# Performance work log

Hardware: AMD Instinct MI355X
Metric: run time of the kernel (lower is better)

The kernel has to match this reference:

```python
import jax, jax.numpy as jnp
import numpy as np

N = 200000   # nodes
E = 400000   # edges
G = 4096     # graphs in batch
F_IN = 77    # atom feature dim
D = 128      # dim_drug
L = 3        # layer_drug
BN_EPS = 1e-5


def setup_inputs() -> dict:
    key = jax.random.key(0)
    ks = jax.random.split(key, 16)
    inp = {}
    inp["x"] = jax.random.normal(ks[0], (N, F_IN), jnp.float32)
    inp["edge_index"] = jax.random.randint(ks[1], (2, E), 0, N, dtype=jnp.int64)
    inp["batch"] = jnp.sort(jax.random.randint(ks[2], (N,), 0, G, dtype=jnp.int64))
    dims = [F_IN, D, D]
    i = 3
    for l in range(L):
        din = dims[l]
        inp[f"w1_{l}"] = jax.random.normal(ks[i], (din, D), jnp.float32) / np.sqrt(din); i += 1
        inp[f"b1_{l}"] = jnp.zeros((D,), jnp.float32)
        inp[f"w2_{l}"] = jax.random.normal(ks[i], (D, D), jnp.float32) / np.sqrt(D); i += 1
        inp[f"b2_{l}"] = jnp.zeros((D,), jnp.float32)
        inp[f"gamma_{l}"] = jnp.ones((D,), jnp.float32)
        inp[f"beta_{l}"] = jnp.zeros((D,), jnp.float32)
    inp["w_emb"] = jax.random.normal(ks[i], (L * D, 256), jnp.float32) / np.sqrt(L * D)
    inp["b_emb"] = jnp.zeros((256,), jnp.float32)
    return inp


def _gin_bn_layer(h, src, dst, w1, b1, w2, b2, gamma, beta):
    # GINConv (eps=0): out_i = MLP(x_i + sum_{j->i} x_j)
    agg = jax.ops.segment_sum(h[src], dst, num_segments=N)  # scatter-add aggregation
    h = h + agg
    h = jax.nn.relu(h @ w1 + b1) @ w2 + b2                  # GIN MLP
    h = jax.nn.relu(h)                                       # outer F.relu
    mu = jnp.mean(h, axis=0)
    var = jnp.var(h, axis=0)                                  # biased var (training-mode BN)
    return (h - mu) * jax.lax.rsqrt(var + BN_EPS) * gamma + beta


def reference(x, edge_index, batch,
              w1_0, b1_0, w2_0, b2_0, gamma_0, beta_0,
              w1_1, b1_1, w2_1, b2_1, gamma_1, beta_1,
              w1_2, b1_2, w2_2, b2_2, gamma_2, beta_2,
              w_emb, b_emb):
    src, dst = edge_index[0], edge_index[1]
    layers = [(w1_0, b1_0, w2_0, b2_0, gamma_0, beta_0),
              (w1_1, b1_1, w2_1, b2_1, gamma_1, beta_1),
              (w1_2, b1_2, w2_2, b2_2, gamma_2, beta_2)]
    h = x
    outs = []
    for (w1, b1, w2, b2, g, b) in layers:
        h = _gin_bn_layer(h, src, dst, w1, b1, w2, b2, g, b)
        outs.append(h)
    node_rep = jnp.concatenate(outs, axis=1)                  # JK 'cat' -> [N, L*D]
    pooled = jax.ops.segment_max(node_rep, batch, num_segments=G)  # global_max_pool -> [G, L*D]
    # drug_emb: Linear -> ReLU -> Dropout (identity in eval)
    return jax.nn.relu(pooled @ w_emb + b_emb)
```

## Files before the change

### kernel.cpp

```cpp
#include <hip/hip_runtime.h>
#include <hip/hip_bf16.h>
#include <float.h>

#define NN 200000
#define NE 400000
#define NG 4096
#define FIN 77
#define DD 128
#define BN_EPS 1e-5f
#define NB_SCAN ((NN + 255) / 256)
#define NBLK (NN / 64)

typedef float f32x4 __attribute__((ext_vector_type(4)));
typedef short s16x8 __attribute__((ext_vector_type(8)));

__device__ __forceinline__ unsigned short f2bf(float x) {
    unsigned b = __float_as_uint(x);
    unsigned r = (b + 0x7FFFu + ((b >> 16) & 1u)) >> 16;
    return (unsigned short)r;
}
__device__ __forceinline__ float bf2f(unsigned short u) {
    return __uint_as_float(((unsigned)u) << 16);
}

__global__ void detect_kernel(const unsigned* eidx, const unsigned* batch, int* flags) {
    if (threadIdx.x == 0 && blockIdx.x == 0) {
        int e64 = 1, b64 = 1;
        for (int i = 0; i < 16; i++) {
            if (eidx[2 * NE - 1 - 2 * i] != 0u) e64 = 0;
            if (batch[NN - 1 - 2 * i] != 0u) b64 = 0;
        }
        flags[0] = e64;
        flags[1] = b64;
    }
}

__device__ __forceinline__ int load_idx(const void* p, int is64, long long i) {
    return is64 ? (int)((const long long*)p)[i] : ((const int*)p)[i];
}

__global__ void graph_starts_kernel(const void* batch, const int* flags, int* start) {
    int g = blockIdx.x * blockDim.x + threadIdx.x;
    if (g > NG) return;
    int is64 = flags[1];
    int lo = 0, hi = NN;
    while (lo < hi) {
        int mid = (lo + hi) >> 1;
        int v = load_idx(batch, is64, mid);
        if (v < g) lo = mid + 1; else hi = mid;
    }
    start[g] = lo;
}

__global__ void count_kernel(const void* __restrict__ eidx, const int* __restrict__ flags,
                             int* __restrict__ deg) {
    int e = blockIdx.x * 256 + threadIdx.x;
    if (e >= NE) return;
    int dst = load_idx(eidx, flags[0], (long long)NE + e);
    atomicAdd(&deg[dst], 1);
}

__global__ void scan1_kernel(const int* __restrict__ deg, int* __restrict__ incl,
                             int* __restrict__ bsum) {
    __shared__ int sh[256];
    int i = blockIdx.x * 256 + threadIdx.x;
    int v = (i < NN) ? deg[i] : 0;
    sh[threadIdx.x] = v;
    __syncthreads();
    for (int off = 1; off < 256; off <<= 1) {
        int t = (threadIdx.x >= off) ? sh[threadIdx.x - off] : 0;
        __syncthreads();
        sh[threadIdx.x] += t;
        __syncthreads();
    }
    if (i < NN) incl[i] = sh[threadIdx.x];
    if (threadIdx.x == 255) bsum[blockIdx.x] = sh[255];
}

__global__ void scan2_kernel(int* __restrict__ bsum) {
    __shared__ int sh[NB_SCAN];
    for (int i = threadIdx.x; i < NB_SCAN; i += blockDim.x) sh[i] = bsum[i];
    __syncthreads();
    if (threadIdx.x == 0) {
        int acc = 0;
        for (int i = 0; i < NB_SCAN; i++) { int t = sh[i]; sh[i] = acc; acc += t; }
    }
    __syncthreads();
    for (int i = threadIdx.x; i < NB_SCAN; i += blockDim.x) bsum[i] = sh[i];
}

__global__ void scan3_kernel(const int* __restrict__ incl, const int* __restrict__ deg,
                             const int* __restrict__ bsum, int* __restrict__ rowptr,
                             int* __restrict__ cursor) {
    int i = blockIdx.x * 256 + threadIdx.x;
    if (i < NN) {
        int ex = bsum[blockIdx.x] + incl[i] - deg[i];
        rowptr[i] = ex;
        cursor[i] = ex;
    }
    if (i == 0) rowptr[NN] = NE;
}

__global__ void fill_kernel(const void* __restrict__ eidx, const int* __restrict__ flags,
                            int* __restrict__ cursor, int* __restrict__ slots) {
    int e = blockIdx.x * 256 + threadIdx.x;
    if (e >= NE) return;
    int is64 = flags[0];
    int src = load_idx(eidx, is64, e);
    int dst = load_idx(eidx, is64, (long long)NE + e);
    int pos = atomicAdd(&cursor[dst], 1);
    slots[pos] = src;
}

__global__ void xconv_kernel(const float* __restrict__ x, unsigned short* __restrict__ xb) {
    int idx = blockIdx.x * 256 + threadIdx.x;
    int row = idx / 12, c8 = (idx % 12) * 8;
    union { s16x8 v; unsigned short u[8]; } pk;
#pragma unroll
    for (int j = 0; j < 8; j++) {
        int c = c8 + j;
        pk.u[j] = (c < FIN) ? f2bf(x[(long long)row * FIN + c]) : (unsigned short)0;
    }
    *(s16x8*)&xb[(long long)row * 96 + c8] = pk.v;
}

__global__ void wconv_kernel(const float* __restrict__ w1, const float* __restrict__ w2,
                             unsigned short* __restrict__ wt1, unsigned short* __restrict__ wt2,
                             int K1) {
    int idx = blockIdx.x * 256 + threadIdx.x;
    int c = idx >> 7, k = idx & 127;
    wt1[idx] = f2bf(k < K1 ? w1[k * DD + c] : 0.f);
    wt2[idx] = f2bf(w2[k * DD + c]);
}

template <int L0>
__global__ __launch_bounds__(256) void fused_layer(
    const unsigned short* __restrict__ src, const float* __restrict__ ss,
    const int* __restrict__ rowptr, const int* __restrict__ slots,
    const unsigned short* __restrict__ wt1, const unsigned short* __restrict__ wt2,
    const float* __restrict__ b1, const float* __restrict__ b2,
    unsigned short* __restrict__ out, float* __restrict__ partials)
{
    __shared__ unsigned short Xs[64 * 128];
    constexpr int SK = L0 ? 96 : 128;
    constexpr int KS1 = L0 ? 3 : 4;
    int tid = threadIdx.x;
    int lane = tid & 63;
    int w = tid >> 6;
    long long rowBase = (long long)blockIdx.x * 64;

    {
        int rp = tid >> 4;
        int ci = tid & 15;
        int c8 = ci * 8;
        float sc[8], sh[8];
        if (!L0) {
#pragma unroll
            for (int j = 0; j < 8; j++) { sc[j] = ss[c8 + j]; sh[j] = ss[DD + c8 + j]; }
        }
#pragma unroll
        for (int p = 0; p < 4; p++) {
            int r = p * 16 + rp;
            long long gr = rowBase + r;
            float a[8];
            if (L0 && c8 >= 96) {
#pragma unroll
                for (int j = 0; j < 8; j++) a[j] = 0.f;
            } else {
                int lo = rowptr[gr], hi = rowptr[gr + 1];
                s16x8 v = *(const s16x8*)&src[gr * SK + c8];
                if (L0) {
#pragma unroll
                    for (int j = 0; j < 8; j++) a[j] = bf2f((unsigned short)v[j]);
                } else {
#pragma unroll
                    for (int j = 0; j < 8; j++) a[j] = bf2f((unsigned short)v[j]) * sc[j] + sh[j];
                }
                int k = lo;
                for (; k + 1 < hi; k += 2) {
                    long long s0 = slots[k], s1 = slots[k + 1];
                    s16x8 v0 = *(const s16x8*)&src[s0 * SK + c8];
                    s16x8 v1 = *(const s16x8*)&src[s1 * SK + c8];
                    if (L0) {
#pragma unroll
                        for (int j = 0; j < 8; j++)
                            a[j] += bf2f((unsigned short)v0[j]) + bf2f((unsigned short)v1[j]);
                    } else {
#pragma unroll
                        for (int j = 0; j < 8; j++)
                            a[j] += (bf2f((unsigned short)v0[j]) * sc[j] + sh[j]) +
                                    (bf2f((unsigned short)v1[j]) * sc[j] + sh[j]);
                    }
                }
                if (k < hi) {
                    long long s0 = slots[k];
                    s16x8 v0 = *(const s16x8*)&src[s0 * SK + c8];
#pragma unroll
                    for (int j = 0; j < 8; j++) {
                        float f = bf2f((unsigned short)v0[j]);
                        a[j] += L0 ? f : (f * sc[j] + sh[j]);
                    }
                }
            }
            union { s16x8 v; unsigned short u[8]; } pk;
#pragma unroll
            for (int j = 0; j < 8; j++) pk.u[j] = f2bf(a[j]);
            *(s16x8*)&Xs[r * 128 + (c8 ^ ((r & 7) << 3))] = pk.v;
        }
    }

    int colbase = w * 32 + (lane & 15);
    s16x8 w1f[2][4], w2f[2][4];
#pragma unroll
    for (int cb = 0; cb < 2; cb++) {
        int col = colbase + cb * 16;
#pragma unroll
        for (int ks = 0; ks < KS1; ks++)
            w1f[cb][ks] = *(const s16x8*)&wt1[col * 128 + ks * 32 + (lane >> 4) * 8];
#pragma unroll
        for (int ks = 0; ks < 4; ks++)
            w2f[cb][ks] = *(const s16x8*)&wt2[col * 128 + ks * 32 + (lane >> 4) * 8];
    }
    float bs1[2], bs2[2];
#pragma unroll
    for (int cb = 0; cb < 2; cb++) {
        bs1[cb] = b1[colbase + cb * 16];
        bs2[cb] = b2[colbase + cb * 16];
    }

    __syncthreads();

    f32x4 acc[4][2];
#pragma unroll
    for (int rb = 0; rb < 4; rb++)
#pragma unroll
        for (int cb = 0; cb < 2; cb++) acc[rb][cb] = 0;
#pragma unroll
    for (int ks = 0; ks < KS1; ks++) {
        int lk = ks * 32 + (lane >> 4) * 8;
        s16x8 af[4];
#pragma unroll
        for (int rb = 0; rb < 4; rb++) {
            int r = rb * 16 + (lane & 15);
            af[rb] = *(const s16x8*)&Xs[r * 128 + (lk ^ ((r & 7) << 3))];
        }
#pragma unroll
        for (int rb = 0; rb < 4; rb++)
#pragma unroll
            for (int cb = 0; cb < 2; cb++)
                acc[rb][cb] = __builtin_amdgcn_mfma_f32_16x16x32_bf16(af[rb], w1f[cb][ks], acc[rb][cb], 0, 0, 0);
    }

    __syncthreads();

#pragma unroll
    for (int rb = 0; rb < 4; rb++)
#pragma unroll
        for (int cb = 0; cb < 2; cb++) {
            int col = colbase + cb * 16;
#pragma unroll
            for (int reg = 0; reg < 4; reg++) {
                int row = rb * 16 + (lane >> 4) * 4 + reg;
                float v = fmaxf(acc[rb][cb][reg] + bs1[cb], 0.f);
                Xs[row * 128 + (col ^ ((row & 7) << 3))] = f2bf(v);
            }
        }

    __syncthreads();

#pragma unroll
    for (int rb = 0; rb < 4; rb++)
#pragma unroll
        for (int cb = 0; cb < 2; cb++) acc[rb][cb] = 0;
#pragma unroll
    for (int ks = 0; ks < 4; ks++) {
        int lk = ks * 32 + (lane >> 4) * 8;
        s16x8 af[4];
#pragma unroll
        for (int rb = 0; rb < 4; rb++) {
            int r = rb * 16 + (lane & 15);
            af[rb] = *(const s16x8*)&Xs[r * 128 + (lk ^ ((r & 7) << 3))];
        }
#pragma unroll
        for (int rb = 0; rb < 4; rb++)
#pragma unroll
            for (int cb = 0; cb < 2; cb++)
                acc[rb][cb] = __builtin_amdgcn_mfma_f32_16x16x32_bf16(af[rb], w2f[cb][ks], acc[rb][cb], 0, 0, 0);
    }

    float ps[2] = {0.f, 0.f}, pq[2] = {0.f, 0.f};
#pragma unroll
    for (int rb = 0; rb < 4; rb++)
#pragma unroll
        for (int cb = 0; cb < 2; cb++) {
            int col = colbase + cb * 16;
#pragma unroll
            for (int reg = 0; reg < 4; reg++) {
                long long row = rowBase + rb * 16 + (lane >> 4) * 4 + reg;
                float v = fmaxf(acc[rb][cb][reg] + bs2[cb], 0.f);
                unsigned short ub = f2bf(v);
                out[row * DD + col] = ub;
                float vb = bf2f(ub);
                ps[cb] += vb;
                pq[cb] += vb * vb;
            }
        }
#pragma unroll
    for (int cb = 0; cb < 2; cb++) {
        ps[cb] += __shfl_xor(ps[cb], 16); ps[cb] += __shfl_xor(ps[cb], 32);
        pq[cb] += __shfl_xor(pq[cb], 16); pq[cb] += __shfl_xor(pq[cb], 32);
        if (lane < 16) {
            int col = colbase + cb * 16;
            partials[(long long)blockIdx.x * 256 + col] = ps[cb];
            partials[(long long)blockIdx.x * 256 + 128 + col] = pq[cb];
        }
    }
}

__global__ void bn_red2_kernel(const float* __restrict__ partials, float* __restrict__ sums) {
    float s = 0.f;
    for (int b = blockIdx.x; b < NBLK; b += gridDim.x)
        s += partials[(long long)b * 256 + threadIdx.x];
    atomicAdd(&sums[threadIdx.x], s);
}

__global__ void bn_finalize_kernel(const float* __restrict__ sums,
                                   const float* __restrict__ gamma,
                                   const float* __restrict__ beta,
                                   float* __restrict__ ss) {
    int c = threadIdx.x;
    float mu = sums[c] / (float)NN;
    float var = sums[DD + c] / (float)NN - mu * mu;
    float sc = gamma[c] * rsqrtf(var + BN_EPS);
    ss[c] = sc;
    ss[DD + c] = beta[c] - mu * sc;
}

__global__ void pool_kernel(const unsigned short* __restrict__ hm, const float* __restrict__ ss,
                            const int* __restrict__ start, float* __restrict__ pooled, int l) {
    int g = blockIdx.x;
    int c = threadIdx.x;
    int lo = start[g], hi = start[g + 1];
    float sc = ss[c], sh = ss[DD + c];
    float m = -FLT_MAX;
    for (int n = lo; n < hi; n++)
        m = fmaxf(m, bf2f(hm[(long long)n * DD + c]) * sc + sh);
    pooled[(long long)g * (3 * DD) + l * DD + c] = m;
}

__global__ __launch_bounds__(256) void emb_kernel(const float* __restrict__ pooled,
                                                  const float* __restrict__ w,
                                                  const float* __restrict__ b,
                                                  float* __restrict__ out) {
    __shared__ float pl[8][384];
    int tid = threadIdx.x;
    int g0 = blockIdx.x * 8;
#pragma unroll
    for (int i = 0; i < 12; i++) {
        int idx = tid + i * 256;
        int gg = idx / 384, c = idx % 384;
        pl[gg][c] = pooled[(long long)(g0 + gg) * 384 + c];
    }
    __syncthreads();
    float acc[8];
#pragma unroll
    for (int gg = 0; gg < 8; gg++) acc[gg] = 0.f;
    for (int k = 0; k < 384; k++) {
        float wv = w[k * 256 + tid];
#pragma unroll
        for (int gg = 0; gg < 8; gg++) acc[gg] += pl[gg][k] * wv;
    }
    float bb = b[tid];
#pragma unroll
    for (int gg = 0; gg < 8; gg++)
        out[(long long)(g0 + gg) * 256 + tid] = fmaxf(acc[gg] + bb, 0.f);
}

extern "C" void kernel_launch(void* const* d_in, const int* in_sizes, int n_in,
                              void* d_out, int out_size, void* d_ws, size_t ws_size,
                              hipStream_t stream) {
    const float* x = (const float*)d_in[0];
    const void* eidx = d_in[1];
    const void* batch = d_in[2];
    const float* w1[3] = { (const float*)d_in[3],  (const float*)d_in[9],  (const float*)d_in[15] };
    const float* b1[3] = { (const float*)d_in[4],  (const float*)d_in[10], (const float*)d_in[16] };
    const float* w2[3] = { (const float*)d_in[5],  (const float*)d_in[11], (const float*)d_in[17] };
    const float* b2[3] = { (const float*)d_in[6],  (const float*)d_in[12], (const float*)d_in[18] };
    const float* gm[3] = { (const float*)d_in[7],  (const float*)d_in[13], (const float*)d_in[19] };
    const float* bt[3] = { (const float*)d_in[8],  (const float*)d_in[14], (const float*)d_in[20] };
    const float* w_emb = (const float*)d_in[21];
    const float* b_emb = (const float*)d_in[22];
    float* out = (float*)d_out;

    unsigned short* R1 = (unsigned short*)d_ws;
    unsigned short* R2 = R1 + (size_t)NN * DD;
    float* pooled = (float*)(R2 + (size_t)NN * DD);
    float* partials = pooled + (size_t)NG * 384;
    unsigned short* wtb = (unsigned short*)(partials + (size_t)NBLK * 256);
    float* sums = (float*)(wtb + 6 * 16384);
    float* ss = sums + 256;
    int* start = (int*)(ss + 256);
    int* flags = start + NG + 1;
    int* deg = flags + 2;
    int* incl = deg + NN;
    int* bsum = incl + NN;
    int* rowptr = bsum + NB_SCAN;
    int* cursor = rowptr + NN + 1;
    int* slots = cursor + NN;

    detect_kernel<<<1, 64, 0, stream>>>((const unsigned*)eidx, (const unsigned*)batch, flags);
    graph_starts_kernel<<<(NG + 1 + 255) / 256, 256, 0, stream>>>(batch, flags, start);

    hipMemsetAsync(deg, 0, (size_t)NN * sizeof(int), stream);
    count_kernel<<<(NE + 255) / 256, 256, 0, stream>>>(eidx, flags, deg);
    scan1_kernel<<<NB_SCAN, 256, 0, stream>>>(deg, incl, bsum);
    scan2_kernel<<<1, 1024, 0, stream>>>(bsum);
    scan3_kernel<<<NB_SCAN, 256, 0, stream>>>(incl, deg, bsum, rowptr, cursor);
    fill_kernel<<<(NE + 255) / 256, 256, 0, stream>>>(eidx, flags, cursor, slots);

    xconv_kernel<<<(NN * 12) / 256, 256, 0, stream>>>(x, R1);
    for (int l = 0; l < 3; l++)
        wconv_kernel<<<64, 256, 0, stream>>>(w1[l], w2[l], wtb + l * 2 * 16384,
                                             wtb + l * 2 * 16384 + 16384, (l == 0) ? FIN : DD);

    unsigned short* hin[3] = { R1, R2, R1 };
    unsigned short* hout[3] = { R2, R1, R2 };
    for (int l = 0; l < 3; l++) {
        const unsigned short* wt1 = wtb + l * 2 * 16384;
        const unsigned short* wt2 = wt1 + 16384;
        if (l == 0)
            fused_layer<1><<<NBLK, 256, 0, stream>>>(hin[l], ss, rowptr, slots, wt1, wt2,
                                                     b1[l], b2[l], hout[l], partials);
        else
            fused_layer<0><<<NBLK, 256, 0, stream>>>(hin[l], ss, rowptr, slots, wt1, wt2,
                                                     b1[l], b2[l], hout[l], partials);
        hipMemsetAsync(sums, 0, 256 * sizeof(float), stream);
        bn_red2_kernel<<<64, 256, 0, stream>>>(partials, sums);
        bn_finalize_kernel<<<1, 128, 0, stream>>>(sums, gm[l], bt[l], ss);
        pool_kernel<<<NG, 128, 0, stream>>>(hout[l], ss, start, pooled, l);
    }
    emb_kernel<<<NG / 8, 256, 0, stream>>>(pooled, w_emb, b_emb, out);
}
```

Baseline: 438.3 us.

## Fuse global max pooling into layer epilogue via atomic per-graph max/min

Removes the separate pool kernel and graph-start binary search. Each fused layer now tracks per-graph running max, plus min when any gamma is negative, of the post-ReLU bf16 values and merges them with integer atomics. A small finalize kernel then applies the BN affine, picking max or min by the sign of the scale. The last layer skips writing its hidden output since only the pooled values are needed. Aggregation is also changed to sum raw bf16 neighbours and apply the BN affine once, scaled by the neighbour count, and bn_red2 gets more blocks. The cost is extra memsets and atomic traffic per layer.

```diff
diff --git a/kernel.cpp b/kernel.cpp
--- a/kernel.cpp
+++ b/kernel.cpp
@@ -39,17 +39,11 @@
     return is64 ? (int)((const long long*)p)[i] : ((const int*)p)[i];
 }
 
-__global__ void graph_starts_kernel(const void* batch, const int* flags, int* start) {
-    int g = blockIdx.x * blockDim.x + threadIdx.x;
-    if (g > NG) return;
-    int is64 = flags[1];
-    int lo = 0, hi = NN;
-    while (lo < hi) {
-        int mid = (lo + hi) >> 1;
-        int v = load_idx(batch, is64, mid);
-        if (v < g) lo = mid + 1; else hi = mid;
-    }
-    start[g] = lo;
+__global__ void gsign_kernel(const float* ga, const float* gb, const float* gc, int* gneg) {
+    int c = threadIdx.x;
+    if (ga[c] < 0.f) atomicOr(&gneg[0], 1);
+    if (gb[c] < 0.f) atomicOr(&gneg[1], 1);
+    if (gc[c] < 0.f) atomicOr(&gneg[2], 1);
 }
 
 __global__ void count_kernel(const void* __restrict__ eidx, const int* __restrict__ flags,
@@ -133,15 +127,18 @@
     wt2[idx] = f2bf(w2[k * DD + c]);
 }
 
-template <int L0>
+template <int L0, int STOREH>
 __global__ __launch_bounds__(256) void fused_layer(
     const unsigned short* __restrict__ src, const float* __restrict__ ss,
     const int* __restrict__ rowptr, const int* __restrict__ slots,
     const unsigned short* __restrict__ wt1, const unsigned short* __restrict__ wt2,
     const float* __restrict__ b1, const float* __restrict__ b2,
-    unsigned short* __restrict__ out, float* __restrict__ partials)
+    unsigned short* __restrict__ out, float* __restrict__ partials,
+    const int* __restrict__ flags, const void* __restrict__ batch,
+    const int* __restrict__ gneg_l, float* __restrict__ pmax, float* __restrict__ pmin)
 {
     __shared__ unsigned short Xs[64 * 128];
+    __shared__ int gidL[64];
     constexpr int SK = L0 ? 96 : 128;
     constexpr int KS1 = L0 ? 3 : 4;
     int tid = threadIdx.x;
@@ -149,10 +146,11 @@
     int w = tid >> 6;
     long long rowBase = (long long)blockIdx.x * 64;
 
+    if (tid < 64) gidL[tid] = load_idx(batch, flags[1], rowBase + tid);
+
     {
         int rp = tid >> 4;
-        int ci = tid & 15;
-        int c8 = ci * 8;
+        int c8 = (tid & 15) * 8;
         float sc[8], sh[8];
         if (!L0) {
 #pragma unroll
@@ -168,38 +166,27 @@
                 for (int j = 0; j < 8; j++) a[j] = 0.f;
             } else {
                 int lo = rowptr[gr], hi = rowptr[gr + 1];
-                s16x8 v = *(const s16x8*)&src[gr * SK + c8];
-                if (L0) {
-#pragma unroll
-                    for (int j = 0; j < 8; j++) a[j] = bf2f((unsigned short)v[j]);
-                } else {
-#pragma unroll
-                    for (int j = 0; j < 8; j++) a[j] = bf2f((unsigned short)v[j]) * sc[j] + sh[j];
+                int d = hi - lo;
+                long long s0 = (d > 0) ? (long long)slots[lo] : gr;
+                long long s1 = (d > 1) ? (long long)slots[lo + 1] : gr;
+                s16x8 vo = *(const s16x8*)&src[gr * SK + c8];
+                s16x8 v0 = *(const s16x8*)&src[s0 * SK + c8];
+                s16x8 v1 = *(const s16x8*)&src[s1 * SK + c8];
+                float m0 = (d > 0) ? 1.f : 0.f, m1 = (d > 1) ? 1.f : 0.f;
+#pragma unroll
+                for (int j = 0; j < 8; j++)
+                    a[j] = bf2f((unsigned short)vo[j]) + m0 * bf2f((unsigned short)v0[j])
+                                                      + m1 * bf2f((unsigned short)v1[j]);
+                for (int k = lo + 2; k < hi; k++) {
+                    long long sk = slots[k];
+                    s16x8 vk = *(const s16x8*)&src[sk * SK + c8];
+#pragma unroll
+                    for (int j = 0; j < 8; j++) a[j] += bf2f((unsigned short)vk[j]);
                 }
-                int k = lo;
-                for (; k + 1 < hi; k += 2) {
-                    long long s0 = slots[k], s1 = slots[k + 1];
-                    s16x8 v0 = *(const s16x8*)&src[s0 * SK + c8];
-                    s16x8 v1 = *(const s16x8*)&src[s1 * SK + c8];
-                    if (L0) {
-#pragma unroll
-                        for (int j = 0; j < 8; j++)
-                            a[j] += bf2f((unsigned short)v0[j]) + bf2f((unsigned short)v1[j]);
-                    } else {
-#pragma unroll
-                        for (int j = 0; j < 8; j++)
-                            a[j] += (bf2f((unsigned short)v0[j]) * sc[j] + sh[j]) +
-                                    (bf2f((unsigned short)v1[j]) * sc[j] + sh[j]);
-                    }
-                }
-                if (k < hi) {
-                    long long s0 = slots[k];
-                    s16x8 v0 = *(const s16x8*)&src[s0 * SK + c8];
-#pragma unroll
-                    for (int j = 0; j < 8; j++) {
-                        float f = bf2f((unsigned short)v0[j]);
-                        a[j] += L0 ? f : (f * sc[j] + sh[j]);
-                    }
+                if (!L0) {
+                    float cnt = (float)(d + 1);
+#pragma unroll
+                    for (int j = 0; j < 8; j++) a[j] = a[j] * sc[j] + cnt * sh[j];
                 }
             }
             union { s16x8 v; unsigned short u[8]; } pk;
@@ -288,23 +275,39 @@
                 acc[rb][cb] = __builtin_amdgcn_mfma_f32_16x16x32_bf16(af[rb], w2f[cb][ks], acc[rb][cb], 0, 0, 0);
     }
 
+    int gn = gneg_l[0];
     float ps[2] = {0.f, 0.f}, pq[2] = {0.f, 0.f};
 #pragma unroll
-    for (int rb = 0; rb < 4; rb++)
-#pragma unroll
-        for (int cb = 0; cb < 2; cb++) {
-            int col = colbase + cb * 16;
+    for (int cb = 0; cb < 2; cb++) {
+        int col = colbase + cb * 16;
+        int curg = -1;
+        float cmx = 0.f, cmn = 0.f;
+#pragma unroll
+        for (int rb = 0; rb < 4; rb++) {
 #pragma unroll
             for (int reg = 0; reg < 4; reg++) {
-                long long row = rowBase + rb * 16 + (lane >> 4) * 4 + reg;
+                int lr = rb * 16 + (lane >> 4) * 4 + reg;
                 float v = fmaxf(acc[rb][cb][reg] + bs2[cb], 0.f);
                 unsigned short ub = f2bf(v);
-                out[row * DD + col] = ub;
+                if (STOREH) out[(rowBase + lr) * DD + col] = ub;
                 float vb = bf2f(ub);
-                ps[cb] += vb;
-                pq[cb] += vb * vb;
+                ps[cb] += vb; pq[cb] += vb * vb;
+                int g = gidL[lr];
+                if (g != curg) {
+                    if (curg >= 0) {
+                        atomicMax((int*)&pmax[(long long)curg * DD + col], __float_as_int(cmx));
+                        if (gn) atomicMin((int*)&pmin[(long long)curg * DD + col], __float_as_int(cmn));
+                    }
+                    curg = g; cmx = vb; cmn = vb;
+                } else {
+                    cmx = fmaxf(cmx, vb);
+                    cmn = fminf(cmn, vb);
+                }
             }
         }
+        atomicMax((int*)&pmax[(long long)curg * DD + col], __float_as_int(cmx));
+        if (gn) atomicMin((int*)&pmin[(long long)curg * DD + col], __float_as_int(cmn));
+    }
 #pragma unroll
     for (int cb = 0; cb < 2; cb++) {
         ps[cb] += __shfl_xor(ps[cb], 16); ps[cb] += __shfl_xor(ps[cb], 32);
@@ -336,16 +339,13 @@
     ss[DD + c] = beta[c] - mu * sc;
 }
 
-__global__ void pool_kernel(const unsigned short* __restrict__ hm, const float* __restrict__ ss,
-                            const int* __restrict__ start, float* __restrict__ pooled, int l) {
-    int g = blockIdx.x;
-    int c = threadIdx.x;
-    int lo = start[g], hi = start[g + 1];
+__global__ void pool_fin_kernel(const float* __restrict__ pmax, const float* __restrict__ pmin,
+                                const float* __restrict__ ss, float* __restrict__ pooled, int l) {
+    int idx = blockIdx.x * 256 + threadIdx.x;
+    int g = idx >> 7, c = idx & 127;
     float sc = ss[c], sh = ss[DD + c];
-    float m = -FLT_MAX;
-    for (int n = lo; n < hi; n++)
-        m = fmaxf(m, bf2f(hm[(long long)n * DD + c]) * sc + sh);
-    pooled[(long long)g * (3 * DD) + l * DD + c] = m;
+    float v = (sc >= 0.f) ? (sc * pmax[idx] + sh) : (sc * pmin[idx] + sh);
+    pooled[(long long)g * (3 * DD) + l * DD + c] = v;
 }
 
 __global__ __launch_bounds__(256) void emb_kernel(const float* __restrict__ pooled,
@@ -396,12 +396,14 @@
     unsigned short* R2 = R1 + (size_t)NN * DD;
     float* pooled = (float*)(R2 + (size_t)NN * DD);
     float* partials = pooled + (size_t)NG * 384;
-    unsigned short* wtb = (unsigned short*)(partials + (size_t)NBLK * 256);
+    float* pmax = partials + (size_t)NBLK * 256;
+    float* pmin = pmax + (size_t)NG * DD;
+    unsigned short* wtb = (unsigned short*)(pmin + (size_t)NG * DD);
     float* sums = (float*)(wtb + 6 * 16384);
     float* ss = sums + 256;
-    int* start = (int*)(ss + 256);
-    int* flags = start + NG + 1;
-    int* deg = flags + 2;
+    int* gneg = (int*)(ss + 256);
+    int* flags = gneg + 4;
+    int* deg = flags + 4;
     int* incl = deg + NN;
     int* bsum = incl + NN;
     int* rowptr = bsum + NB_SCAN;
@@ -409,7 +411,8 @@
     int* slots = cursor + NN;
 
     detect_kernel<<<1, 64, 0, stream>>>((const unsigned*)eidx, (const unsigned*)batch, flags);
-    graph_starts_kernel<<<(NG + 1 + 255) / 256, 256, 0, stream>>>(batch, flags, start);
+    hipMemsetAsync(gneg, 0, 4 * sizeof(int), stream);
+    gsign_kernel<<<1, 128, 0, stream>>>(gm[0], gm[1], gm[2], gneg);
 
     hipMemsetAsync(deg, 0, (size_t)NN * sizeof(int), stream);
     count_kernel<<<(NE + 255) / 256, 256, 0, stream>>>(eidx, flags, deg);
@@ -428,16 +431,24 @@
     for (int l = 0; l < 3; l++) {
         const unsigned short* wt1 = wtb + l * 2 * 16384;
         const unsigned short* wt2 = wt1 + 16384;
+        hipMemsetAsync(pmax, 0x00, (size_t)NG * DD * sizeof(float), stream);
+        hipMemsetAsync(pmin, 0x7F, (size_t)NG * DD * sizeof(float), stream);
+        hipMemsetAsync(sums, 0, 256 * sizeof(float), stream);
         if (l == 0)
-            fused_layer<1><<<NBLK, 256, 0, stream>>>(hin[l], ss, rowptr, slots, wt1, wt2,
-                                                     b1[l], b2[l], hout[l], partials);
+            fused_layer<1, 1><<<NBLK, 256, 0, stream>>>(hin[l], ss, rowptr, slots, wt1, wt2,
+                                                        b1[l], b2[l], hout[l], partials,
+                                                        flags, batch, gneg + l, pmax, pmin);
+        else if (l == 1)
+            fused_layer<0, 1><<<NBLK, 256, 0, stream>>>(hin[l], ss, rowptr, slots, wt1, wt2,
+                                                        b1[l], b2[l], hout[l], partials,
+                                                        flags, batch, gneg + l, pmax, pmin);
         else
-            fused_layer<0><<<NBLK, 256, 0, stream>>>(hin[l], ss, rowptr, slots, wt1, wt2,
-                                                     b1[l], b2[l], hout[l], partials);
-        hipMemsetAsync(sums, 0, 256 * sizeof(float), stream);
-        bn_red2_kernel<<<64, 256, 0, stream>>>(partials, sums);
+            fused_layer<0, 0><<<NBLK, 256, 0, stream>>>(hin[l], ss, rowptr, slots, wt1, wt2,
+                                                        b1[l], b2[l], hout[l], partials,
+                                                        flags, batch, gneg + l, pmax, pmin);
+        bn_red2_kernel<<<256, 256, 0, stream>>>(partials, sums);
         bn_finalize_kernel<<<1, 128, 0, stream>>>(sums, gm[l], bt[l], ss);
-        pool_kernel<<<NG, 128, 0, stream>>>(hout[l], ss, start, pooled, l);
+        pool_fin_kernel<<<(NG * DD) / 256, 256, 0, stream>>>(pmax, pmin, ss, pooled, l);
     }
     emb_kernel<<<NG / 8, 256, 0, stream>>>(pooled, w_emb, b_emb, out);
 }
```

Result: slower. 460.5 us (+5.1%).
